# Kernel optimization log

Measured on AMD Instinct MI355X. Metric: run time of the kernel, lower is better.

## Reference

```python
import jax, jax.numpy as jnp
import numpy as np

BN_EPS = 1e-5


def binarize(x):
    # sign binarization with straight-through estimator (identity grad)
    return x + jax.lax.stop_gradient(jnp.sign(x) - x)


def conv2d(x, w, stride):
    # x: [N,C,H,W], w: [O,I,kh,kw], VALID padding (PyTorch default padding=0)
    return jax.lax.conv_general_dilated(
        x, w, window_strides=(stride, stride), padding='VALID',
        dimension_numbers=('NCHW', 'OIHW', 'NCHW'))


def batchnorm(x, gamma, beta, mean, var):
    inv = gamma / jnp.sqrt(var + BN_EPS)          # [C]
    return x * inv[None, :, None, None] + (beta - mean * inv)[None, :, None, None]


def setup_inputs() -> dict:
    key = jax.random.key(0)
    ks = jax.random.split(key, 20)
    B = 8192
    f32 = jnp.float32
    d = {
        'x': jax.random.normal(ks[0], (B, 1, 24, 54), f32),
        'conv1_w': jax.random.normal(ks[1], (32, 1, 3, 3), f32) * 0.3,
        'conv1_b': jax.random.normal(ks[2], (32,), f32) * 0.1,
        'bn1_gamma': 1.0 + 0.1 * jax.random.normal(ks[3], (32,), f32),
        'bn1_beta': 0.1 * jax.random.normal(ks[4], (32,), f32),
        'bn1_mean': 0.1 * jax.random.normal(ks[5], (32,), f32),
        'bn1_var': jax.random.uniform(ks[6], (32,), f32, 0.5, 1.5),
        'conv2_w': jax.random.normal(ks[7], (64, 32, 3, 3), f32) * 0.1,
        'conv2_b': jax.random.normal(ks[8], (64,), f32) * 0.1,
        'bn2_gamma': 1.0 + 0.1 * jax.random.normal(ks[9], (64,), f32),
        'bn2_beta': 0.1 * jax.random.normal(ks[10], (64,), f32),
        'bn2_mean': 0.1 * jax.random.normal(ks[11], (64,), f32),
        'bn2_var': jax.random.uniform(ks[12], (64,), f32, 0.5, 1.5),
        'lin_w': jax.random.normal(ks[13], (500, 3840), f32) * 0.02,
        'lin_b': jax.random.normal(ks[14], (500,), f32) * 0.1,
        'out_w': jax.random.normal(ks[15], (10, 500), f32) * 0.05,
        'out_b': jax.random.normal(ks[16], (10,), f32) * 0.1,
    }
    return d


def reference(x, conv1_w, conv1_b, bn1_gamma, bn1_beta, bn1_mean, bn1_var,
              conv2_w, conv2_b, bn2_gamma, bn2_beta, bn2_mean, bn2_var,
              lin_w, lin_b, out_w, out_b):
    # conv1: input channels (1) != 3 -> input binarized; weight binarized; float bias
    h = conv2d(binarize(x), binarize(conv1_w), 2) + conv1_b[None, :, None, None]
    h = jax.nn.relu(batchnorm(h, bn1_gamma, bn1_beta, bn1_mean, bn1_var))  # [B,32,11,26]
    # conv2: input channels (32) != 3 -> input binarized (values in {0,1} post-ReLU)
    h = conv2d(binarize(h), binarize(conv2_w), 2) + conv2_b[None, :, None, None]
    h = jax.nn.relu(batchnorm(h, bn2_gamma, bn2_beta, bn2_mean, bn2_var))  # [B,64,5,12]
    h = h.reshape(-1, 3840)
    # BinarizeLinear: in_features (3840, 500) != 784 -> input binarized
    h = jax.nn.relu(binarize(h) @ binarize(lin_w).T + lin_b[None, :])      # [B,500]
    y = binarize(h) @ binarize(out_w).T + out_b[None, :]                   # [B,10]
    return y
```

## Files before the change

### kernel.cpp

```cpp
#include <hip/hip_runtime.h>
#include <cstdint>

#define BN_EPS 1e-5f

static constexpr int NB = 8192;
static constexpr int JLIN = 500;

typedef int v4i  __attribute__((ext_vector_type(4)));
typedef int v16i __attribute__((ext_vector_type(16)));


__global__ __launch_bounds__(256) void pack_kernel(
    const float* __restrict__ conv1_w, const float* __restrict__ conv1_b,
    const float* __restrict__ conv2_w, const float* __restrict__ conv2_b,
    const float* __restrict__ lin_w, const float* __restrict__ lin_b,
    const float* __restrict__ out_w,
    const float* __restrict__ bn1_g, const float* __restrict__ bn1_b,
    const float* __restrict__ bn1_m, const float* __restrict__ bn1_v,
    const float* __restrict__ bn2_g, const float* __restrict__ bn2_b,
    const float* __restrict__ bn2_m, const float* __restrict__ bn2_v,
    uint4* __restrict__ wbfrag, uint32_t* __restrict__ cdat,
    uint32_t* __restrict__ lut, uint32_t* __restrict__ wout,
    int* __restrict__ Tlin, uint4* __restrict__ wcfrag)
{
    __shared__ float    s_c1w[288];
    __shared__ uint32_t s_wp[32];
    __shared__ float    s_inv1[32], s_sh1[32], s_b1[32];

    int tid = threadIdx.x;
    int b   = blockIdx.x;

    if (b < 512) {
        int e  = b * 256 + tid;
        int L  = e & 63;
        int kq = (e >> 6) & 127;
        int jt = e >> 13;
        int j  = jt * 32 + (L & 31);
        int h  = L >> 5;
        uint32_t dd[4] = {0u, 0u, 0u, 0u};
        if (j < JLIN) {
            int c  = kq >> 1, hi = kq & 1;
            int nb = (hi ? 28 : 32) - 16 * h;
            const float* src = lin_w + (size_t)j * 3840 + c * 60 + hi * 32 + 16 * h;
            #pragma unroll
            for (int i = 0; i < 16; ++i) {
                uint32_t byte = 0;
                if (i < nb) byte = (src[i] > 0.0f) ? 0x01u : 0xFFu;
                dd[i >> 2] |= byte << (8 * (i & 3));
            }
        }
        wbfrag[e] = make_uint4(dd[0], dd[1], dd[2], dd[3]);
        return;
    }

    if (b >= 520) {
        int e = (b - 520) * 256 + tid;
        if (e < 1152) {
            int t = e >> 7;
            int n = (e >> 6) & 1;
            int L = e & 63;
            int c = n * 32 + (L & 31);
            int hb = L >> 5;
            bool flip = (bn2_g[c] < 0.0f);
            uint32_t dd[4] = {0u, 0u, 0u, 0u};
            #pragma unroll
            for (int i = 0; i < 16; ++i) {
                int ic = 16 * hb + i;
                float w = conv2_w[c * 288 + ic * 9 + t];
                uint32_t byte = ((w > 0.0f) == flip) ? 0xFFu : 0x01u;
                dd[i >> 2] |= byte << (8 * (i & 3));
            }
            wcfrag[e] = make_uint4(dd[0], dd[1], dd[2], dd[3]);
        }
        return;
    }

    int mb = b - 512;
    if (mb < 2) {
        for (int i = tid; i < 288; i += 256) s_c1w[i] = conv1_w[i];
        __syncthreads();
        if (tid < 32) {
            uint32_t wp = 0;
            for (int t = 0; t < 9; ++t)
                wp |= (s_c1w[tid * 9 + t] < 0.0f ? 1u : 0u) << t;
            s_wp[tid] = wp;
            float inv = bn1_g[tid] / sqrtf(bn1_v[tid] + BN_EPS);
            s_inv1[tid] = inv;
            s_sh1[tid]  = bn1_b[tid] - bn1_m[tid] * inv;
            s_b1[tid]   = conv1_b[tid];
        }
        __syncthreads();
        uint32_t px = (uint32_t)(mb * 256 + tid);
        uint32_t word = 0;
        for (int c = 0; c < 32; ++c) {
            int d = 9 - 2 * __popc(px ^ s_wp[c]);
            float z = __fadd_rn((float)d, s_b1[c]);
            z = __fadd_rn(__fmul_rn(z, s_inv1[c]), s_sh1[c]);
            word |= (z > 0.0f ? 1u : 0u) << c;
        }
        lut[px] = word;
        return;
    }

    int idx = (mb - 2) * 256 + tid;
    if (idx < 576) {
        int c = idx / 9, tap = idx % 9;
        uint32_t w = 0;
        for (int ic = 0; ic < 32; ++ic)
            w |= (conv2_w[c * 288 + ic * 9 + tap] > 0.0f ? 1u : 0u) << ic;
        float inv = bn2_g[c] / sqrtf(bn2_v[c] + BN_EPS);
        if (inv < 0.0f) w = ~w;
        cdat[tap * 64 + c] = w;
    } else if (idx < 576 + 64) {
        int c = idx - 576;
        float inv = bn2_g[c] / sqrtf(bn2_v[c] + BN_EPS);
        float sh  = bn2_b[c] - bn2_m[c] * inv;
        float b2  = conv2_b[c];
        int T = 10000;
        for (int u = -300; u <= 300; ++u) {
            float v = (inv < 0.0f) ? (float)(-u) : (float)u;
            float z = __fadd_rn(__fmul_rn(__fadd_rn(v, b2), inv), sh);
            if (z > 0.0f) { T = u; break; }
        }
        cdat[576 + c] = (uint32_t)T;
    } else if (idx < 576 + 64 + 512) {
        int j = idx - (576 + 64);
        int T = 10000;
        if (j < JLIN) {
            float lb = lin_b[j];
            int base = (int)floorf(-lb) - 2;
            for (int u = base; u <= base + 5; ++u)
                if (__fadd_rn((float)u, lb) > 0.0f) { T = u; break; }
        }
        Tlin[j] = T;
    } else if (idx < 576 + 64 + 512 + 160) {
        int t = idx - (576 + 64 + 512);
        int j = t >> 4, k = t & 15;
        uint32_t w = 0;
        for (int bb = 0; bb < 32; ++bb) {
            int jj = k * 32 + bb;
            if (jj < JLIN) w |= (out_w[j * 500 + jj] > 0.0f ? 1u : 0u) << bb;
        }
        wout[t] = w;
    }
}

__global__ __launch_bounds__(256) void conv_kernel(
    const float* __restrict__ x,
    const uint32_t* __restrict__ cdat,
    const uint32_t* __restrict__ lut,
    const uint4* __restrict__ wcfrag,
    uint32_t* __restrict__ h2b)
{
    __shared__ uint32_t s_lut[512];
    __shared__ __align__(8) uint32_t s_flat[4][44];
    __shared__ uint32_t s_words[4][288];
    __shared__ uint64_t s_bal[4][2][2][16];

    int tid  = threadIdx.x;
    int lane = tid & 63;
    int wv   = tid >> 6;
    int s    = blockIdx.x * 4 + wv;

    s_lut[tid]       = lut[tid];
    s_lut[tid + 256] = lut[tid + 256];
    __syncthreads();

    const float* xs = x + (size_t)s * 1296;
    float xv[21];
    #pragma unroll
    for (int it = 0; it < 21; ++it) {
        int f = it * 64 + lane;
        xv[it] = (f < 1296) ? xs[f] : 1.0f;
    }
    #pragma unroll
    for (int it = 0; it < 21; ++it) {
        uint64_t mk = __ballot(xv[it] < 0.0f);
        if (lane == 0) *(uint64_t*)&s_flat[wv][2 * it] = mk;
    }
    asm volatile("s_waitcnt lgkmcnt(0)" ::: "memory");
    __builtin_amdgcn_sched_barrier(0);

    #pragma unroll
    for (int ii = 0; ii < 5; ++ii) {
        int wnd = ii * 64 + lane;
        if (wnd < 286) {
            int oy = wnd / 26, ox = wnd - 26 * oy;
            uint32_t pxb = 0;
            #pragma unroll
            for (int ky = 0; ky < 3; ++ky) {
                int bitpos = 54 * (2 * oy + ky) + 2 * ox;
                int d = bitpos >> 5, sh = bitpos & 31;
                uint64_t wp = (uint64_t)s_flat[wv][d] |
                              ((uint64_t)s_flat[wv][d + 1] << 32);
                pxb |= (((uint32_t)(wp >> sh)) & 7u) << (3 * ky);
            }
            s_words[wv][wnd] = s_lut[pxb];
        }
    }
    asm volatile("s_waitcnt lgkmcnt(0)" ::: "memory");
    __builtin_amdgcn_sched_barrier(0);

    int row32 = lane & 31;
    int hb    = lane >> 5;
    int sh_hb = 16 * hb;
    int p1v   = 32 + row32; if (p1v > 59) p1v = 59;
    int wb0, wb1;
    { int oy = row32 / 12, ox = row32 - 12 * oy; wb0 = 52 * oy + 2 * ox; }
    { int oy = p1v / 12,   ox = p1v - 12 * oy;   wb1 = 52 * oy + 2 * ox; }

    v16i acc[2][2] = {};
    #pragma unroll
    for (int t = 0; t < 9; ++t) {
        const int koff = (t / 3) * 26 + (t % 3);
        uint4 b0 = wcfrag[t * 128 + lane];
        uint4 b1 = wcfrag[t * 128 + 64 + lane];
        v4i bf0 = {(int)b0.x, (int)b0.y, (int)b0.z, (int)b0.w};
        v4i bf1 = {(int)b1.x, (int)b1.y, (int)b1.z, (int)b1.w};
        #pragma unroll
        for (int rt = 0; rt < 2; ++rt) {
            uint32_t w  = s_words[wv][(rt ? wb1 : wb0) + koff];
            uint32_t hw = w >> sh_hb;
            v4i af;
            af[0] = (int)((((hw      ) & 0xFu) * 0x204081u) & 0x01010101u);
            af[1] = (int)((((hw >> 4 ) & 0xFu) * 0x204081u) & 0x01010101u);
            af[2] = (int)((((hw >> 8 ) & 0xFu) * 0x204081u) & 0x01010101u);
            af[3] = (int)((((hw >> 12) & 0xFu) * 0x204081u) & 0x01010101u);
            acc[rt][0] = __builtin_amdgcn_mfma_i32_32x32x32_i8(af, bf0, acc[rt][0], 0, 0, 0);
            acc[rt][1] = __builtin_amdgcn_mfma_i32_32x32x32_i8(af, bf1, acc[rt][1], 0, 0, 0);
        }
    }

    int T0 = (int)cdat[576 + row32];
    int T1 = (int)cdat[576 + 32 + row32];
    #pragma unroll
    for (int rt = 0; rt < 2; ++rt) {
        #pragma unroll
        for (int r = 0; r < 16; ++r) {
            uint64_t m0 = __ballot(acc[rt][0][r] >= T0);
            uint64_t m1 = __ballot(acc[rt][1][r] >= T1);
            if (lane == 0) {
                s_bal[wv][rt][0][r] = m0;
                s_bal[wv][rt][1][r] = m1;
            }
        }
    }
    asm volatile("s_waitcnt lgkmcnt(0)" ::: "memory");
    __builtin_amdgcn_sched_barrier(0);

    {
        int n  = lane >> 5, cc = lane & 31;
        uint32_t w0 = 0, w1 = 0;
        #pragma unroll
        for (int rt = 0; rt < 2; ++rt) {
            #pragma unroll
            for (int r = 0; r < 16; ++r) {
                const int base = (r & 3) + 8 * (r >> 2);
                uint64_t m = s_bal[wv][rt][n][r];
                uint32_t b0 = (uint32_t)(m >> cc) & 1u;
                uint32_t b1 = (uint32_t)(m >> (cc + 32)) & 1u;
                const int p0 = rt * 32 + base;
                const int p1 = p0 + 4;
                if (p0 < 32) w0 |= b0 << p0; else w1 |= b0 << (p0 - 32);
                if (p1 < 60) {
                    if (p1 < 32) w0 |= b1 << p1; else w1 |= b1 << (p1 - 32);
                }
            }
        }
        *(uint2*)(h2b + (size_t)s * 128 + 2 * lane) = make_uint2(w0, w1);
    }
}

__global__ __launch_bounds__(256) void lin2_kernel(
    const uint32_t* __restrict__ h2b,
    const uint4* __restrict__ wbfrag,
    const int* __restrict__ Tlin,
    uint32_t* __restrict__ h3w)
{
    __shared__ uint8_t As[32 * 520];

    int tid  = threadIdx.x;
    int lane = tid & 63;
    int wv   = __builtin_amdgcn_readfirstlane((int)(tid >> 6));
    int sblk = blockIdx.x >> 2;
    int jgrp = blockIdx.x & 3;
    int jt   = jgrp * 4 + wv;
    int s0   = sblk * 32;

    int T = Tlin[jt * 32 + (lane & 31)];
    int row  = lane & 31;
    int half = lane >> 5;

    v16i acc = {};

    for (int chunk = 0; chunk < 8; ++chunk) {
        #pragma unroll
        for (int ii = 0; ii < 2; ++ii) {
            int e = ii * 256 + tid;
            int sm = e >> 4, wl = e & 15;
            uint32_t w = h2b[(size_t)(s0 + sm) * 128 + chunk * 16 + wl];
            uint32_t dw[8];
            #pragma unroll
            for (int q = 0; q < 8; ++q)
                dw[q] = (((w >> (4 * q)) & 0xFu) * 0x204081u) & 0x01010101u;
            uint64_t* dst = (uint64_t*)(As + sm * 520 + wl * 32);
            dst[0] = (uint64_t)dw[0] | ((uint64_t)dw[1] << 32);
            dst[1] = (uint64_t)dw[2] | ((uint64_t)dw[3] << 32);
            dst[2] = (uint64_t)dw[4] | ((uint64_t)dw[5] << 32);
            dst[3] = (uint64_t)dw[6] | ((uint64_t)dw[7] << 32);
        }
        __syncthreads();

        const uint4* bsrc = wbfrag + ((size_t)jt * 128 + chunk * 16) * 64 + lane;
        #pragma unroll 4
        for (int kq = 0; kq < 16; ++kq) {
            uint4 bw = bsrc[kq * 64];
            v4i bf = {(int)bw.x, (int)bw.y, (int)bw.z, (int)bw.w};
            const uint8_t* ap = As + row * 520 + kq * 32 + half * 16;
            uint64_t lo0 = *(const uint64_t*)ap;
            uint64_t hi0 = *(const uint64_t*)(ap + 8);
            v4i a0 = {(int)(uint32_t)lo0, (int)(lo0 >> 32),
                      (int)(uint32_t)hi0, (int)(hi0 >> 32)};
            acc = __builtin_amdgcn_mfma_i32_32x32x32_i8(a0, bf, acc, 0, 0, 0);
        }
        __syncthreads();
    }

    #pragma unroll
    for (int r = 0; r < 16; ++r) {
        int row0 = (r & 3) + 8 * (r >> 2);
        uint64_t mk = __ballot(acc[r] >= T);
        if (lane == 0) {
            h3w[(size_t)(s0 + row0) * 16 + jt]     = (uint32_t)mk;
            h3w[(size_t)(s0 + row0 + 4) * 16 + jt] = (uint32_t)(mk >> 32);
        }
    }
}

__global__ __launch_bounds__(256) void out_kernel(
    const uint32_t* __restrict__ h3w,
    const uint32_t* __restrict__ wout,
    const float* __restrict__ out_b,
    float* __restrict__ out)
{
    int s = blockIdx.x * 256 + threadIdx.x;
    const uint4* hp = (const uint4*)(h3w + (size_t)s * 16);
    uint4 q0 = hp[0], q1 = hp[1], q2 = hp[2], q3 = hp[3];
    uint32_t w[16] = {q0.x, q0.y, q0.z, q0.w, q1.x, q1.y, q1.z, q1.w,
                      q2.x, q2.y, q2.z, q2.w, q3.x, q3.y, q3.z, q3.w};
    int B = 0;
    #pragma unroll
    for (int k = 0; k < 16; ++k) B += __popc(w[k]);
    #pragma unroll
    for (int o = 0; o < 10; ++o) {
        int P = 0;
        #pragma unroll
        for (int k = 0; k < 16; ++k) P += __popc(w[k] & wout[o * 16 + k]);
        out[(size_t)s * 10 + o] = __fadd_rn((float)(2 * P - B), out_b[o]);
    }
}

extern "C" void kernel_launch(void* const* d_in, const int* in_sizes, int n_in,
                              void* d_out, int out_size, void* d_ws, size_t ws_size,
                              hipStream_t stream)
{
    const float* x       = (const float*)d_in[0];
    const float* conv1_w = (const float*)d_in[1];
    const float* conv1_b = (const float*)d_in[2];
    const float* bn1_g   = (const float*)d_in[3];
    const float* bn1_b   = (const float*)d_in[4];
    const float* bn1_m   = (const float*)d_in[5];
    const float* bn1_v   = (const float*)d_in[6];
    const float* conv2_w = (const float*)d_in[7];
    const float* conv2_b = (const float*)d_in[8];
    const float* bn2_g   = (const float*)d_in[9];
    const float* bn2_b   = (const float*)d_in[10];
    const float* bn2_m   = (const float*)d_in[11];
    const float* bn2_v   = (const float*)d_in[12];
    const float* lin_w   = (const float*)d_in[13];
    const float* lin_b   = (const float*)d_in[14];
    const float* out_w   = (const float*)d_in[15];
    const float* out_b   = (const float*)d_in[16];

    char* ws = (char*)d_ws;
    uint32_t* h2b    = (uint32_t*)(ws + 0);
    uint4*    wbfrag = (uint4*)   (ws + 4194304);
    uint32_t* h3w    = (uint32_t*)(ws + 6291456);
    uint32_t* cdat   = (uint32_t*)(ws + 6815744);
    uint32_t* lut    = (uint32_t*)(ws + 6818304);
    uint32_t* wout   = (uint32_t*)(ws + 6820352);
    int*      Tlin   = (int*)     (ws + 6820992);
    uint4*    wcfrag = (uint4*)   (ws + 6855808);

    pack_kernel<<<525, 256, 0, stream>>>(conv1_w, conv1_b, conv2_w, conv2_b,
                                         lin_w, lin_b, out_w,
                                         bn1_g, bn1_b, bn1_m, bn1_v,
                                         bn2_g, bn2_b, bn2_m, bn2_v,
                                         wbfrag, cdat, lut, wout, Tlin, wcfrag);
    conv_kernel<<<NB / 4, 256, 0, stream>>>(x, cdat, lut, wcfrag, h2b);
    lin2_kernel<<<1024, 256, 0, stream>>>(h2b, wbfrag, Tlin, h3w);
    out_kernel<<<32, 256, 0, stream>>>(h3w, wout, out_b, (float*)d_out);
}
```

Baseline: 170.7 us.

## Pack conv thresholds via lane shuffle and prefetch next h2b chunk in lin2

In the conv kernel, the ballot-and-LDS round trip used to build the packed h2 bit words is replaced. Each lane now builds its own bits from the MFMA accumulator and exchanges half of them with lane^32 through a shuffle, which removes the shared-memory buffer and its wait. In the lin2 kernel, the h2b word for the next chunk is loaded into a register after the barrier, so the global load overlaps the MFMA loop of the current chunk. This keeps two extra registers live and depends on the accumulator layout being mapped correctly for the new bit packing.

```diff
diff --git a/kernel.cpp b/kernel.cpp
--- a/kernel.cpp
+++ b/kernel.cpp
@@ -155,7 +155,6 @@
     __shared__ uint32_t s_lut[512];
     __shared__ __align__(8) uint32_t s_flat[4][44];
     __shared__ uint32_t s_words[4][288];
-    __shared__ uint64_t s_bal[4][2][2][16];
 
     int tid  = threadIdx.x;
     int lane = tid & 63;
@@ -231,42 +230,27 @@
         }
     }
 
-    int T0 = (int)cdat[576 + row32];
-    int T1 = (int)cdat[576 + 32 + row32];
-    #pragma unroll
-    for (int rt = 0; rt < 2; ++rt) {
-        #pragma unroll
-        for (int r = 0; r < 16; ++r) {
-            uint64_t m0 = __ballot(acc[rt][0][r] >= T0);
-            uint64_t m1 = __ballot(acc[rt][1][r] >= T1);
-            if (lane == 0) {
-                s_bal[wv][rt][0][r] = m0;
-                s_bal[wv][rt][1][r] = m1;
-            }
-        }
-    }
-    asm volatile("s_waitcnt lgkmcnt(0)" ::: "memory");
-    __builtin_amdgcn_sched_barrier(0);
-
     {
-        int n  = lane >> 5, cc = lane & 31;
-        uint32_t w0 = 0, w1 = 0;
+        int T0 = (int)cdat[576 + row32];
+        int T1 = (int)cdat[576 + 32 + row32];
+        uint32_t w_rt[2];
         #pragma unroll
         for (int rt = 0; rt < 2; ++rt) {
+            uint32_t lw0 = 0, lw1 = 0;
             #pragma unroll
             for (int r = 0; r < 16; ++r) {
-                const int base = (r & 3) + 8 * (r >> 2);
-                uint64_t m = s_bal[wv][rt][n][r];
-                uint32_t b0 = (uint32_t)(m >> cc) & 1u;
-                uint32_t b1 = (uint32_t)(m >> (cc + 32)) & 1u;
-                const int p0 = rt * 32 + base;
-                const int p1 = p0 + 4;
-                if (p0 < 32) w0 |= b0 << p0; else w1 |= b0 << (p0 - 32);
-                if (p1 < 60) {
-                    if (p1 < 32) w0 |= b1 << p1; else w1 |= b1 << (p1 - 32);
-                }
+                const uint32_t pb = 1u << ((r & 3) + 8 * (r >> 2));
+                if (acc[rt][0][r] >= T0) lw0 |= pb;
+                if (acc[rt][1][r] >= T1) lw1 |= pb;
             }
-        }
+            lw0 <<= 4 * hb;
+            lw1 <<= 4 * hb;
+            uint32_t send = hb ? lw0 : lw1;
+            uint32_t recv = (uint32_t)__shfl_xor((int)send, 32);
+            w_rt[rt] = recv | (hb ? lw1 : lw0);
+        }
+        uint32_t w0 = w_rt[0];
+        uint32_t w1 = w_rt[1] & 0x0FFFFFFFu;
         *(uint2*)(h2b + (size_t)s * 128 + 2 * lane) = make_uint2(w0, w1);
     }
 }
@@ -291,25 +275,41 @@
     int row  = lane & 31;
     int half = lane >> 5;
 
+    int sm0 = tid >> 4,        wl0 = tid & 15;
+    int sm1 = (256 + tid) >> 4, wl1 = tid & 15;
+    const uint32_t* src0 = h2b + (size_t)(s0 + sm0) * 128 + wl0;
+    const uint32_t* src1 = h2b + (size_t)(s0 + sm1) * 128 + wl1;
+
     v16i acc = {};
+    uint32_t wreg0 = src0[0];
+    uint32_t wreg1 = src1[0];
 
     for (int chunk = 0; chunk < 8; ++chunk) {
-        #pragma unroll
-        for (int ii = 0; ii < 2; ++ii) {
-            int e = ii * 256 + tid;
-            int sm = e >> 4, wl = e & 15;
-            uint32_t w = h2b[(size_t)(s0 + sm) * 128 + chunk * 16 + wl];
+        {
             uint32_t dw[8];
             #pragma unroll
             for (int q = 0; q < 8; ++q)
-                dw[q] = (((w >> (4 * q)) & 0xFu) * 0x204081u) & 0x01010101u;
-            uint64_t* dst = (uint64_t*)(As + sm * 520 + wl * 32);
+                dw[q] = (((wreg0 >> (4 * q)) & 0xFu) * 0x204081u) & 0x01010101u;
+            uint64_t* dst = (uint64_t*)(As + sm0 * 520 + wl0 * 32);
             dst[0] = (uint64_t)dw[0] | ((uint64_t)dw[1] << 32);
             dst[1] = (uint64_t)dw[2] | ((uint64_t)dw[3] << 32);
             dst[2] = (uint64_t)dw[4] | ((uint64_t)dw[5] << 32);
             dst[3] = (uint64_t)dw[6] | ((uint64_t)dw[7] << 32);
+            #pragma unroll
+            for (int q = 0; q < 8; ++q)
+                dw[q] = (((wreg1 >> (4 * q)) & 0xFu) * 0x204081u) & 0x01010101u;
+            dst = (uint64_t*)(As + sm1 * 520 + wl1 * 32);
+            dst[0] = (uint64_t)dw[0] | ((uint64_t)dw[1] << 32);
+            dst[1] = (uint64_t)dw[2] | ((uint64_t)dw[3] << 32);
+            dst[2] = (uint64_t)dw[4] | ((uint64_t)dw[5] << 32);
+            dst[3] = (uint64_t)dw[6] | ((uint64_t)dw[7] << 32);
         }
         __syncthreads();
+
+        if (chunk < 7) {
+            wreg0 = src0[(chunk + 1) * 16];
+            wreg1 = src1[(chunk + 1) * 16];
+        }
 
         const uint4* bsrc = wbfrag + ((size_t)jt * 128 + chunk * 16) * 64 + lane;
         #pragma unroll 4
```

Measured after the change: 161.5 us. 1.06x faster.
